# Kernel tuning notes

Measured on AMD Instinct MI355X. Metric: run time of the kernel, lower is better.

The kernel has to match this reference:

```python
import jax, jax.numpy as jnp
import numpy as np

D_MODEL = 1024
NUM_HEADS = 16
MAX_SEQ_LEN = 2048
THETA = 10000.0
D_K = D_MODEL // NUM_HEADS


def setup_inputs() -> dict:
    key = jax.random.key(0)
    ks = jax.random.split(key, 5)
    B, S = 4, MAX_SEQ_LEN
    std = 2.0 / (D_MODEL + D_MODEL)
    x = jax.random.normal(ks[0], (B, S, D_MODEL), dtype=jnp.float32)
    Wq = jax.random.normal(ks[1], (D_MODEL, D_MODEL), dtype=jnp.float32) * std
    Wk = jax.random.normal(ks[2], (D_MODEL, D_MODEL), dtype=jnp.float32) * std
    Wv = jax.random.normal(ks[3], (D_MODEL, D_MODEL), dtype=jnp.float32) * std
    Wo = jax.random.normal(ks[4], (D_MODEL, D_MODEL), dtype=jnp.float32) * std
    token_positions = jnp.arange(S, dtype=jnp.int64) if jax.config.jax_enable_x64 else jnp.arange(S, dtype=jnp.int32)
    return {"x": x, "token_positions": token_positions, "Wq": Wq, "Wk": Wk, "Wv": Wv, "Wo": Wo}


def _rope_tables(token_positions):
    # angles[i, j] = pos_i / theta^(2j/d_k),  j in [0, d_k/2)
    k = jnp.arange(0, D_K, 2, dtype=jnp.float32)
    inv_freq = 1.0 / (THETA ** (k / D_K))  # [d_k/2]
    angles = token_positions.astype(jnp.float32)[:, None] * inv_freq[None, :]  # [s, d_k/2]
    return jnp.sin(angles), jnp.cos(angles)


def _apply_rope(x, sin, cos):
    # x: [b, h, s, d_k], sin/cos: [s, d_k/2] broadcast over b,h
    x_even = x[..., 0::2]
    x_odd = x[..., 1::2]
    out_even = x_even * cos - x_odd * sin
    out_odd = x_odd * cos + x_even * sin
    # interleave back: [..., d_k/2, 2] -> [..., d_k]
    return jnp.stack([out_even, out_odd], axis=-1).reshape(x.shape)


def reference(x, token_positions, Wq, Wk, Wv, Wo):
    B, S, _ = x.shape
    H, Dk = NUM_HEADS, D_K

    def proj(W):
        y = jnp.einsum('oi,bsi->bso', W, x)
        return y.reshape(B, S, H, Dk).transpose(0, 2, 1, 3)  # [b, h, s, d_k]

    q, k, v = proj(Wq), proj(Wk), proj(Wv)
    sin, cos = _rope_tables(token_positions)
    q = _apply_rope(q, sin, cos)
    k = _apply_rope(k, sin, cos)

    scores = jnp.einsum('bhqd,bhkd->bhqk', q, k) / jnp.sqrt(jnp.float32(Dk))
    mask = jnp.tril(jnp.ones((S, S), dtype=bool))  # causal
    scores = jnp.where(mask[None, None], scores, -jnp.inf)
    attn = jax.nn.softmax(scores, axis=-1)
    out = jnp.einsum('bhqk,bhkd->bhqd', attn, v)
    out = out.transpose(0, 2, 1, 3).reshape(B, S, H * Dk)
    return jnp.einsum('oi,bsi->bso', Wo, out)
```

## Files before the change

kernel.cpp:

```cpp
#include <hip/hip_runtime.h>
#include <math.h>

#define S_LEN 2048
#define NHEADS 16
#define DK 64

typedef _Float16 h4 __attribute__((ext_vector_type(4)));
typedef _Float16 h8 __attribute__((ext_vector_type(8)));
typedef float f4 __attribute__((ext_vector_type(4)));

__device__ __forceinline__ void glds16(const void* g, void* l) {
  __builtin_amdgcn_global_load_lds(
      (const __attribute__((address_space(1))) unsigned int*)g,
      (__attribute__((address_space(3))) unsigned int*)l, 16, 0, 0);
}

__global__ void rope_table_kernel(const int* __restrict__ pos,
                                  float* __restrict__ sc) {
  int idx = blockIdx.x * blockDim.x + threadIdx.x;
  if (idx >= S_LEN * 32) return;
  int s = idx >> 5, p = idx & 31;
  double inv = pow(10000.0, -(double)(2 * p) / 64.0);
  double a = (double)pos[s] * inv;
  sc[s * 64 + 2 * p]     = (float)sin(a);
  sc[s * 64 + 2 * p + 1] = (float)cos(a);
}

__global__ __launch_bounds__(256) void cvt_all(
    const float* __restrict__ x,
    const float* __restrict__ w0, const float* __restrict__ w1,
    const float* __restrict__ w2, const float* __restrict__ w3,
    _Float16* __restrict__ xh, _Float16* __restrict__ wh) {
  int bid = blockIdx.x;
  if (bid < 8192) {
    int i = bid * 256 + threadIdx.x;
    float4 v = *(const float4*)(x + (size_t)i * 4);
    h4 o = {(_Float16)v.x, (_Float16)v.y, (_Float16)v.z, (_Float16)v.w};
    *(h4*)&xh[(size_t)i * 4] = o;
  } else {
    int j = (bid - 8192) * 256 + threadIdx.x;
    const float* srcs[4] = {w0, w1, w2, w3};
    int which = j >> 18;
    int off = (j & 262143) * 4;
    float4 v = *(const float4*)(srcs[which] + off);
    h4 o = {(_Float16)(v.x * 256.f), (_Float16)(v.y * 256.f),
            (_Float16)(v.z * 256.f), (_Float16)(v.w * 256.f)};
    *(h4*)&wh[(size_t)which * 1048576 + off] = o;
  }
}

__global__ __launch_bounds__(256) void gemm_qkv(
    const _Float16* __restrict__ A, const _Float16* __restrict__ W3,
    _Float16* __restrict__ Qo, _Float16* __restrict__ Ko,
    _Float16* __restrict__ Vto, const float* __restrict__ sc_t) {
  __shared__ _Float16 As[128 * 32];
  __shared__ _Float16 Bs[128 * 32];
  const int t = threadIdx.x;
  const int lane = t & 63;
  const int w = t >> 6;
  const int mat = blockIdx.x >> 3;
  const int n0 = (blockIdx.x & 7) * 128;
  const int m0 = blockIdx.y * 128;
  const _Float16* B = W3 + (size_t)mat * 1048576;
  const int wm = (w >> 1) * 64;
  const int wn = (w & 1) * 64;
  const int lm = lane & 15;
  const int kq = (lane >> 4) * 8;
  const int srow = lane >> 2;
  const int skof = (lane & 3) * 8;

  f4 acc[4][4];
#pragma unroll
  for (int i = 0; i < 4; i++)
#pragma unroll
    for (int j = 0; j < 4; j++) {
      f4 z = {0.f, 0.f, 0.f, 0.f};
      acc[i][j] = z;
    }

  for (int k0 = 0; k0 < 1024; k0 += 32) {
    __syncthreads();
#pragma unroll
    for (int c = 0; c < 2; c++) {
      int rr = (w + c * 4) * 16 + srow;
      glds16(A + (size_t)(m0 + rr) * 1024 + k0 + skof, (char*)As + (w + c * 4) * 1024);
      glds16(B + (size_t)(n0 + rr) * 1024 + k0 + skof, (char*)Bs + (w + c * 4) * 1024);
    }
    __syncthreads();

    h8 af[4], bf[4];
#pragma unroll
    for (int mt = 0; mt < 4; mt++)
      af[mt] = *(const h8*)(As + (wm + mt * 16 + lm) * 32 + kq);
#pragma unroll
    for (int nt = 0; nt < 4; nt++)
      bf[nt] = *(const h8*)(Bs + (wn + nt * 16 + lm) * 32 + kq);
#pragma unroll
    for (int mt = 0; mt < 4; mt++)
#pragma unroll
      for (int nt = 0; nt < 4; nt++)
        acc[mt][nt] = __builtin_amdgcn_mfma_f32_16x16x32_f16(af[mt], bf[nt],
                                                             acc[mt][nt], 0, 0, 0);
  }

  const float scale = 1.0f / 256.0f;
  const int quad = lane >> 4;
#pragma unroll
  for (int mt = 0; mt < 4; mt++) {
#pragma unroll
    for (int nt = 0; nt < 4; nt++) {
      int n = n0 + wn + nt * 16 + lm;
      int d = n & 63, h = n >> 6;
      int mbase = m0 + wm + mt * 16 + quad * 4;
      int s = mbase & (S_LEN - 1), b = mbase >> 11;
      if (mat == 2) {
        h4 ov = {(_Float16)(acc[mt][nt][0] * scale), (_Float16)(acc[mt][nt][1] * scale),
                 (_Float16)(acc[mt][nt][2] * scale), (_Float16)(acc[mt][nt][3] * scale)};
        *(h4*)&Vto[(((size_t)b * NHEADS + h) * DK + d) * S_LEN + s] = ov;
      } else {
        _Float16* C16 = (mat == 0) ? Qo : Ko;
        int p2 = d & ~1;
#pragma unroll
        for (int r = 0; r < 4; r++) {
          float v = acc[mt][nt][r] * scale;
          float2 sc = *(const float2*)&sc_t[(s + r) * 64 + p2];
          float partner = __shfl_xor(v, 1);
          v = (d & 1) ? fmaf(v, sc.y, partner * sc.x)
                      : fmaf(v, sc.y, -partner * sc.x);
          C16[(((size_t)b * NHEADS + h) * S_LEN + (s + r)) * DK + d] = (_Float16)v;
        }
      }
    }
  }
}

__global__ __launch_bounds__(256) void gemm_out(
    const _Float16* __restrict__ A, const _Float16* __restrict__ B,
    float* __restrict__ C32) {
  __shared__ _Float16 As[128 * 32];
  __shared__ _Float16 Bs[128 * 32];
  const int t = threadIdx.x;
  const int lane = t & 63;
  const int w = t >> 6;
  const int n0 = blockIdx.x * 128;
  const int m0 = blockIdx.y * 128;
  const int wm = (w >> 1) * 64;
  const int wn = (w & 1) * 64;
  const int lm = lane & 15;
  const int kq = (lane >> 4) * 8;
  const int srow = lane >> 2;
  const int skof = (lane & 3) * 8;

  f4 acc[4][4];
#pragma unroll
  for (int i = 0; i < 4; i++)
#pragma unroll
    for (int j = 0; j < 4; j++) {
      f4 z = {0.f, 0.f, 0.f, 0.f};
      acc[i][j] = z;
    }

  for (int k0 = 0; k0 < 1024; k0 += 32) {
    __syncthreads();
#pragma unroll
    for (int c = 0; c < 2; c++) {
      int rr = (w + c * 4) * 16 + srow;
      glds16(A + (size_t)(m0 + rr) * 1024 + k0 + skof, (char*)As + (w + c * 4) * 1024);
      glds16(B + (size_t)(n0 + rr) * 1024 + k0 + skof, (char*)Bs + (w + c * 4) * 1024);
    }
    __syncthreads();

    h8 af[4], bf[4];
#pragma unroll
    for (int mt = 0; mt < 4; mt++)
      af[mt] = *(const h8*)(As + (wm + mt * 16 + lm) * 32 + kq);
#pragma unroll
    for (int nt = 0; nt < 4; nt++)
      bf[nt] = *(const h8*)(Bs + (wn + nt * 16 + lm) * 32 + kq);
#pragma unroll
    for (int mt = 0; mt < 4; mt++)
#pragma unroll
      for (int nt = 0; nt < 4; nt++)
        acc[mt][nt] = __builtin_amdgcn_mfma_f32_16x16x32_f16(af[mt], bf[nt],
                                                             acc[mt][nt], 0, 0, 0);
  }

  const float scale = 1.0f / 256.0f;
  const int quad = lane >> 4;
#pragma unroll
  for (int mt = 0; mt < 4; mt++)
#pragma unroll
    for (int nt = 0; nt < 4; nt++) {
      int n = n0 + wn + nt * 16 + lm;
#pragma unroll
      for (int r = 0; r < 4; r++) {
        int m = m0 + wm + mt * 16 + quad * 4 + r;
        C32[(size_t)m * 1024 + n] = acc[mt][nt][r] * scale;
      }
    }
}

__global__ __launch_bounds__(256) void attn_mfma(
    const _Float16* __restrict__ Q, const _Float16* __restrict__ K,
    const _Float16* __restrict__ Vt, _Float16* __restrict__ O) {
  __shared__ _Float16 Ks[64 * 72];
  __shared__ _Float16 Vs[64 * 72];
  __shared__ _Float16 Ps[128 * 72];

  const int bh = blockIdx.x;
  const int qt = (gridDim.y - 1) - blockIdx.y;
  const int q0 = qt * 128;
  const int t = threadIdx.x;
  const int lane = t & 63;
  const int w = t >> 6;
  const int lm = lane & 15;
  const int quad = lane >> 4;
  const size_t qkbase = (size_t)bh * S_LEN * DK;
  const size_t vbase  = (size_t)bh * DK * S_LEN;
  const int srow = t >> 2;
  const int scol = (t & 3) * 16;
  const int wq0 = q0 + w * 32;

  h8 qf[2][2];
#pragma unroll
  for (int nt = 0; nt < 2; nt++)
#pragma unroll
    for (int kc = 0; kc < 2; kc++) {
      h8 v = *(const h8*)(Q + qkbase + (size_t)(wq0 + nt * 16 + lm) * DK +
                          kc * 32 + quad * 8);
#pragma unroll
      for (int j = 0; j < 8; j++) v[j] = v[j] * (_Float16)0.125f;
      qf[nt][kc] = v;
    }

  f4 oacc[4][2];
#pragma unroll
  for (int mt = 0; mt < 4; mt++)
#pragma unroll
    for (int nt = 0; nt < 2; nt++) {
      f4 z = {0.f, 0.f, 0.f, 0.f};
      oacc[mt][nt] = z;
    }
  float m_i[2] = {-INFINITY, -INFINITY};
  float l_i[2] = {0.f, 0.f};

  const int ktmax = 2 * qt + 1;
  const _Float16* kg = K + qkbase + (size_t)srow * DK + scol;
  const _Float16* vg = Vt + vbase + (size_t)srow * S_LEN + scol;
  h8 pk0 = *(const h8*)kg;
  h8 pk1 = *(const h8*)(kg + 8);
  h8 pv0 = *(const h8*)vg;
  h8 pv1 = *(const h8*)(vg + 8);

  for (int kt = 0; kt <= ktmax; kt++) {
    __syncthreads();
    *(h8*)&Ks[srow * 72 + scol] = pk0;
    *(h8*)&Ks[srow * 72 + scol + 8] = pk1;
    *(h8*)&Vs[srow * 72 + scol] = pv0;
    *(h8*)&Vs[srow * 72 + scol + 8] = pv1;
    if (kt < ktmax) {
      const _Float16* kgn = kg + (size_t)(kt + 1) * 64 * DK;
      const _Float16* vgn = vg + (kt + 1) * 64;
      pk0 = *(const h8*)kgn;
      pk1 = *(const h8*)(kgn + 8);
      pv0 = *(const h8*)vgn;
      pv1 = *(const h8*)(vgn + 8);
    }
    __syncthreads();

    if (kt * 64 <= wq0 + 31) {
      f4 s_[4][2];
#pragma unroll
      for (int mt = 0; mt < 4; mt++)
#pragma unroll
        for (int nt = 0; nt < 2; nt++) {
          f4 z = {0.f, 0.f, 0.f, 0.f};
          s_[mt][nt] = z;
        }
#pragma unroll
      for (int kc = 0; kc < 2; kc++) {
        h8 kf[4];
#pragma unroll
        for (int mt = 0; mt < 4; mt++)
          kf[mt] = *(const h8*)&Ks[(mt * 16 + lm) * 72 + kc * 32 + quad * 8];
#pragma unroll
        for (int mt = 0; mt < 4; mt++)
#pragma unroll
          for (int nt = 0; nt < 2; nt++)
            s_[mt][nt] = __builtin_amdgcn_mfma_f32_16x16x32_f16(kf[mt], qf[nt][kc],
                                                                s_[mt][nt], 0, 0, 0);
      }

      if (kt * 64 + 63 > wq0) {
#pragma unroll
        for (int nt = 0; nt < 2; nt++) {
          int srq = wq0 + nt * 16 + lm;
#pragma unroll
          for (int mt = 0; mt < 4; mt++)
#pragma unroll
            for (int r = 0; r < 4; r++)
              if (kt * 64 + mt * 16 + quad * 4 + r > srq) s_[mt][nt][r] = -INFINITY;
        }
      }

#pragma unroll
      for (int nt = 0; nt < 2; nt++) {
        float mx = -INFINITY;
#pragma unroll
        for (int mt = 0; mt < 4; mt++)
#pragma unroll
          for (int r = 0; r < 4; r++) mx = fmaxf(mx, s_[mt][nt][r]);
        mx = fmaxf(mx, __shfl_xor(mx, 16));
        mx = fmaxf(mx, __shfl_xor(mx, 32));
        const bool grow = __any(mx > m_i[nt]);
        const float mnew = grow ? fmaxf(m_i[nt], mx) : m_i[nt];
        float sum = 0.f;
#pragma unroll
        for (int mt = 0; mt < 4; mt++) {
          float p0 = __expf(s_[mt][nt][0] - mnew);
          float p1 = __expf(s_[mt][nt][1] - mnew);
          float p2 = __expf(s_[mt][nt][2] - mnew);
          float p3 = __expf(s_[mt][nt][3] - mnew);
          sum += (p0 + p1) + (p2 + p3);
          h4 pv = {(_Float16)p0, (_Float16)p1, (_Float16)p2, (_Float16)p3};
          *(h4*)&Ps[(w * 32 + nt * 16 + lm) * 72 + mt * 16 + quad * 4] = pv;
        }
        sum += __shfl_xor(sum, 16);
        sum += __shfl_xor(sum, 32);
        if (grow) {
          float alpha = __expf(m_i[nt] - mnew);
          m_i[nt] = mnew;
          l_i[nt] = fmaf(l_i[nt], alpha, sum);
#pragma unroll
          for (int mt = 0; mt < 4; mt++) {
            oacc[mt][nt][0] *= alpha; oacc[mt][nt][1] *= alpha;
            oacc[mt][nt][2] *= alpha; oacc[mt][nt][3] *= alpha;
          }
        } else {
          l_i[nt] += sum;
        }
      }

#pragma unroll
      for (int kc = 0; kc < 2; kc++) {
        h8 vf[4], pf[2];
#pragma unroll
        for (int mt = 0; mt < 4; mt++)
          vf[mt] = *(const h8*)&Vs[(mt * 16 + lm) * 72 + kc * 32 + quad * 8];
#pragma unroll
        for (int nt = 0; nt < 2; nt++)
          pf[nt] = *(const h8*)&Ps[(w * 32 + nt * 16 + lm) * 72 + kc * 32 + quad * 8];
#pragma unroll
        for (int mt = 0; mt < 4; mt++)
#pragma unroll
          for (int nt = 0; nt < 2; nt++)
            oacc[mt][nt] = __builtin_amdgcn_mfma_f32_16x16x32_f16(vf[mt], pf[nt],
                                                                  oacc[mt][nt], 0, 0, 0);
      }
    }
  }

  const int b = bh >> 4, head = bh & 15;
#pragma unroll
  for (int nt = 0; nt < 2; nt++) {
    float inv = 1.0f / l_i[nt];
    int s = wq0 + nt * 16 + lm;
#pragma unroll
    for (int mt = 0; mt < 4; mt++) {
      h4 ov = {(_Float16)(oacc[mt][nt][0] * inv), (_Float16)(oacc[mt][nt][1] * inv),
               (_Float16)(oacc[mt][nt][2] * inv), (_Float16)(oacc[mt][nt][3] * inv)};
      *(h4*)&O[((size_t)b * S_LEN + s) * 1024 + head * 64 + mt * 16 + quad * 4] = ov;
    }
  }
}

extern "C" void kernel_launch(void* const* d_in, const int* in_sizes, int n_in,
                              void* d_out, int out_size, void* d_ws, size_t ws_size,
                              hipStream_t stream) {
  const float* x   = (const float*)d_in[0];
  const int*   pos = (const int*)d_in[1];
  const float* Wq  = (const float*)d_in[2];
  const float* Wk  = (const float*)d_in[3];
  const float* Wv  = (const float*)d_in[4];
  const float* Wo  = (const float*)d_in[5];
  float* out = (float*)d_out;
  (void)in_sizes; (void)n_in; (void)out_size; (void)ws_size;

  const size_t NT = (size_t)4 * S_LEN * 1024;
  _Float16* q16  = (_Float16*)d_ws;
  _Float16* k16  = q16 + NT;
  _Float16* vt16 = k16 + NT;
  _Float16* aoh  = vt16 + NT;
  _Float16* xh   = aoh + NT;
  _Float16* wh   = xh + NT;
  float* sc_t = (float*)(wh + 4 * 1048576);

  rope_table_kernel<<<256, 256, 0, stream>>>(pos, sc_t);
  cvt_all<<<12288, 256, 0, stream>>>(x, Wq, Wk, Wv, Wo, xh, wh);

  gemm_qkv<<<dim3(24, 64), 256, 0, stream>>>(xh, wh, q16, k16, vt16, sc_t);

  attn_mfma<<<dim3(64, S_LEN / 128), 256, 0, stream>>>(q16, k16, vt16, aoh);

  gemm_out<<<dim3(8, 64), 256, 0, stream>>>(aoh, wh + 3145728, out);
}
```

Measured before the change: 277.4 us.

## Fuse rope table into convert kernel, swizzle attention LDS, shrink out-GEMM tile

Folds the rope sin/cos table computation into the conversion kernel as extra blocks, removing one launch. The attention kernel swaps its padded LDS rows (stride 72) for unpadded rows with an XOR swizzle, which shrinks LDS use, and adds an occupancy hint of 5 blocks per CU. The output GEMM moves from 128x128 to 64x128 tiles, doubling the grid to fill more CUs, at the cost of less B-tile reuse. The swizzle has to match exactly between the stores and the MFMA fragment reads.

```diff
diff --git a/kernel.cpp b/kernel.cpp
--- a/kernel.cpp
+++ b/kernel.cpp
@@ -15,29 +15,19 @@
       (__attribute__((address_space(3))) unsigned int*)l, 16, 0, 0);
 }
 
-__global__ void rope_table_kernel(const int* __restrict__ pos,
-                                  float* __restrict__ sc) {
-  int idx = blockIdx.x * blockDim.x + threadIdx.x;
-  if (idx >= S_LEN * 32) return;
-  int s = idx >> 5, p = idx & 31;
-  double inv = pow(10000.0, -(double)(2 * p) / 64.0);
-  double a = (double)pos[s] * inv;
-  sc[s * 64 + 2 * p]     = (float)sin(a);
-  sc[s * 64 + 2 * p + 1] = (float)cos(a);
-}
-
 __global__ __launch_bounds__(256) void cvt_all(
     const float* __restrict__ x,
     const float* __restrict__ w0, const float* __restrict__ w1,
     const float* __restrict__ w2, const float* __restrict__ w3,
-    _Float16* __restrict__ xh, _Float16* __restrict__ wh) {
+    _Float16* __restrict__ xh, _Float16* __restrict__ wh,
+    const int* __restrict__ pos, float* __restrict__ sc) {
   int bid = blockIdx.x;
   if (bid < 8192) {
     int i = bid * 256 + threadIdx.x;
     float4 v = *(const float4*)(x + (size_t)i * 4);
     h4 o = {(_Float16)v.x, (_Float16)v.y, (_Float16)v.z, (_Float16)v.w};
     *(h4*)&xh[(size_t)i * 4] = o;
-  } else {
+  } else if (bid < 12288) {
     int j = (bid - 8192) * 256 + threadIdx.x;
     const float* srcs[4] = {w0, w1, w2, w3};
     int which = j >> 18;
@@ -46,6 +36,13 @@
     h4 o = {(_Float16)(v.x * 256.f), (_Float16)(v.y * 256.f),
             (_Float16)(v.z * 256.f), (_Float16)(v.w * 256.f)};
     *(h4*)&wh[(size_t)which * 1048576 + off] = o;
+  } else {
+    int idx = (bid - 12288) * 256 + threadIdx.x;
+    int s = idx >> 5, p = idx & 31;
+    double inv = pow(10000.0, -(double)(2 * p) / 64.0);
+    double a = (double)pos[s] * inv;
+    sc[s * 64 + 2 * p]     = (float)sin(a);
+    sc[s * 64 + 2 * p + 1] = (float)cos(a);
   }
 }
 
@@ -137,23 +134,23 @@
 __global__ __launch_bounds__(256) void gemm_out(
     const _Float16* __restrict__ A, const _Float16* __restrict__ B,
     float* __restrict__ C32) {
-  __shared__ _Float16 As[128 * 32];
+  __shared__ _Float16 As[64 * 32];
   __shared__ _Float16 Bs[128 * 32];
   const int t = threadIdx.x;
   const int lane = t & 63;
   const int w = t >> 6;
   const int n0 = blockIdx.x * 128;
-  const int m0 = blockIdx.y * 128;
-  const int wm = (w >> 1) * 64;
+  const int m0 = blockIdx.y * 64;
+  const int wm = (w >> 1) * 32;
   const int wn = (w & 1) * 64;
   const int lm = lane & 15;
   const int kq = (lane >> 4) * 8;
   const int srow = lane >> 2;
   const int skof = (lane & 3) * 8;
 
-  f4 acc[4][4];
-#pragma unroll
-  for (int i = 0; i < 4; i++)
+  f4 acc[2][4];
+#pragma unroll
+  for (int i = 0; i < 2; i++)
 #pragma unroll
     for (int j = 0; j < 4; j++) {
       f4 z = {0.f, 0.f, 0.f, 0.f};
@@ -162,23 +159,23 @@
 
   for (int k0 = 0; k0 < 1024; k0 += 32) {
     __syncthreads();
+    glds16(A + (size_t)(m0 + w * 16 + srow) * 1024 + k0 + skof, (char*)As + w * 1024);
 #pragma unroll
     for (int c = 0; c < 2; c++) {
       int rr = (w + c * 4) * 16 + srow;
-      glds16(A + (size_t)(m0 + rr) * 1024 + k0 + skof, (char*)As + (w + c * 4) * 1024);
       glds16(B + (size_t)(n0 + rr) * 1024 + k0 + skof, (char*)Bs + (w + c * 4) * 1024);
     }
     __syncthreads();
 
-    h8 af[4], bf[4];
-#pragma unroll
-    for (int mt = 0; mt < 4; mt++)
+    h8 af[2], bf[4];
+#pragma unroll
+    for (int mt = 0; mt < 2; mt++)
       af[mt] = *(const h8*)(As + (wm + mt * 16 + lm) * 32 + kq);
 #pragma unroll
     for (int nt = 0; nt < 4; nt++)
       bf[nt] = *(const h8*)(Bs + (wn + nt * 16 + lm) * 32 + kq);
 #pragma unroll
-    for (int mt = 0; mt < 4; mt++)
+    for (int mt = 0; mt < 2; mt++)
 #pragma unroll
       for (int nt = 0; nt < 4; nt++)
         acc[mt][nt] = __builtin_amdgcn_mfma_f32_16x16x32_f16(af[mt], bf[nt],
@@ -188,7 +185,7 @@
   const float scale = 1.0f / 256.0f;
   const int quad = lane >> 4;
 #pragma unroll
-  for (int mt = 0; mt < 4; mt++)
+  for (int mt = 0; mt < 2; mt++)
 #pragma unroll
     for (int nt = 0; nt < 4; nt++) {
       int n = n0 + wn + nt * 16 + lm;
@@ -200,12 +197,12 @@
     }
 }
 
-__global__ __launch_bounds__(256) void attn_mfma(
+__global__ __launch_bounds__(256, 5) void attn_mfma(
     const _Float16* __restrict__ Q, const _Float16* __restrict__ K,
     const _Float16* __restrict__ Vt, _Float16* __restrict__ O) {
-  __shared__ _Float16 Ks[64 * 72];
-  __shared__ _Float16 Vs[64 * 72];
-  __shared__ _Float16 Ps[128 * 72];
+  __shared__ _Float16 Ks[64 * 64];
+  __shared__ _Float16 Vs[64 * 64];
+  __shared__ _Float16 Ps[128 * 64];
 
   const int bh = blockIdx.x;
   const int qt = (gridDim.y - 1) - blockIdx.y;
@@ -215,11 +212,19 @@
   const int w = t >> 6;
   const int lm = lane & 15;
   const int quad = lane >> 4;
+  const int l7 = lm & 7;
   const size_t qkbase = (size_t)bh * S_LEN * DK;
   const size_t vbase  = (size_t)bh * DK * S_LEN;
   const int srow = t >> 2;
   const int scol = (t & 3) * 16;
   const int wq0 = q0 + w * 32;
+  const f4 fzero = {0.f, 0.f, 0.f, 0.f};
+
+  const int r7 = srow & 7;
+  const int su0 = ((t & 3) * 2) ^ r7;
+  const int su1 = ((t & 3) * 2 + 1) ^ r7;
+  const int st0 = srow * 64 + su0 * 8;
+  const int st1 = srow * 64 + su1 * 8;
 
   h8 qf[2][2];
 #pragma unroll
@@ -237,10 +242,7 @@
 #pragma unroll
   for (int mt = 0; mt < 4; mt++)
 #pragma unroll
-    for (int nt = 0; nt < 2; nt++) {
-      f4 z = {0.f, 0.f, 0.f, 0.f};
-      oacc[mt][nt] = z;
-    }
+    for (int nt = 0; nt < 2; nt++) oacc[mt][nt] = fzero;
   float m_i[2] = {-INFINITY, -INFINITY};
   float l_i[2] = {0.f, 0.f};
 
@@ -254,10 +256,10 @@
 
   for (int kt = 0; kt <= ktmax; kt++) {
     __syncthreads();
-    *(h8*)&Ks[srow * 72 + scol] = pk0;
-    *(h8*)&Ks[srow * 72 + scol + 8] = pk1;
-    *(h8*)&Vs[srow * 72 + scol] = pv0;
-    *(h8*)&Vs[srow * 72 + scol + 8] = pv1;
+    *(h8*)&Ks[st0] = pk0;
+    *(h8*)&Ks[st1] = pk1;
+    *(h8*)&Vs[st0] = pv0;
+    *(h8*)&Vs[st1] = pv1;
     if (kt < ktmax) {
       const _Float16* kgn = kg + (size_t)(kt + 1) * 64 * DK;
       const _Float16* vgn = vg + (kt + 1) * 64;
@@ -270,24 +272,28 @@
 
     if (kt * 64 <= wq0 + 31) {
       f4 s_[4][2];
-#pragma unroll
-      for (int mt = 0; mt < 4; mt++)
-#pragma unroll
-        for (int nt = 0; nt < 2; nt++) {
-          f4 z = {0.f, 0.f, 0.f, 0.f};
-          s_[mt][nt] = z;
-        }
-#pragma unroll
-      for (int kc = 0; kc < 2; kc++) {
+      {
         h8 kf[4];
 #pragma unroll
         for (int mt = 0; mt < 4; mt++)
-          kf[mt] = *(const h8*)&Ks[(mt * 16 + lm) * 72 + kc * 32 + quad * 8];
+          kf[mt] = *(const h8*)&Ks[(mt * 16 + lm) * 64 + (quad ^ l7) * 8];
 #pragma unroll
         for (int mt = 0; mt < 4; mt++)
 #pragma unroll
           for (int nt = 0; nt < 2; nt++)
-            s_[mt][nt] = __builtin_amdgcn_mfma_f32_16x16x32_f16(kf[mt], qf[nt][kc],
+            s_[mt][nt] = __builtin_amdgcn_mfma_f32_16x16x32_f16(kf[mt], qf[nt][0],
+                                                                fzero, 0, 0, 0);
+      }
+      {
+        h8 kf[4];
+#pragma unroll
+        for (int mt = 0; mt < 4; mt++)
+          kf[mt] = *(const h8*)&Ks[(mt * 16 + lm) * 64 + ((4 + quad) ^ l7) * 8];
+#pragma unroll
+        for (int mt = 0; mt < 4; mt++)
+#pragma unroll
+          for (int nt = 0; nt < 2; nt++)
+            s_[mt][nt] = __builtin_amdgcn_mfma_f32_16x16x32_f16(kf[mt], qf[nt][1],
                                                                 s_[mt][nt], 0, 0, 0);
       }
 
@@ -315,6 +321,7 @@
         const bool grow = __any(mx > m_i[nt]);
         const float mnew = grow ? fmaxf(m_i[nt], mx) : m_i[nt];
         float sum = 0.f;
+        const int prow = (w * 32 + nt * 16 + lm) * 64;
 #pragma unroll
         for (int mt = 0; mt < 4; mt++) {
           float p0 = __expf(s_[mt][nt][0] - mnew);
@@ -323,7 +330,8 @@
           float p3 = __expf(s_[mt][nt][3] - mnew);
           sum += (p0 + p1) + (p2 + p3);
           h4 pv = {(_Float16)p0, (_Float16)p1, (_Float16)p2, (_Float16)p3};
-          *(h4*)&Ps[(w * 32 + nt * 16 + lm) * 72 + mt * 16 + quad * 4] = pv;
+          int pu = ((mt * 2 + (quad >> 1)) ^ l7) * 8 + (quad & 1) * 4;
+          *(h4*)&Ps[prow + pu] = pv;
         }
         sum += __shfl_xor(sum, 16);
         sum += __shfl_xor(sum, 32);
@@ -346,10 +354,11 @@
         h8 vf[4], pf[2];
 #pragma unroll
         for (int mt = 0; mt < 4; mt++)
-          vf[mt] = *(const h8*)&Vs[(mt * 16 + lm) * 72 + kc * 32 + quad * 8];
+          vf[mt] = *(const h8*)&Vs[(mt * 16 + lm) * 64 + ((kc * 4 + quad) ^ l7) * 8];
 #pragma unroll
         for (int nt = 0; nt < 2; nt++)
-          pf[nt] = *(const h8*)&Ps[(w * 32 + nt * 16 + lm) * 72 + kc * 32 + quad * 8];
+          pf[nt] = *(const h8*)&Ps[(w * 32 + nt * 16 + lm) * 64 +
+                                   ((kc * 4 + quad) ^ l7) * 8];
 #pragma unroll
         for (int mt = 0; mt < 4; mt++)
 #pragma unroll
@@ -395,12 +404,11 @@
   _Float16* wh   = xh + NT;
   float* sc_t = (float*)(wh + 4 * 1048576);
 
-  rope_table_kernel<<<256, 256, 0, stream>>>(pos, sc_t);
-  cvt_all<<<12288, 256, 0, stream>>>(x, Wq, Wk, Wv, Wo, xh, wh);
+  cvt_all<<<12544, 256, 0, stream>>>(x, Wq, Wk, Wv, Wo, xh, wh, pos, sc_t);
 
   gemm_qkv<<<dim3(24, 64), 256, 0, stream>>>(xh, wh, q16, k16, vt16, sc_t);
 
   attn_mfma<<<dim3(64, S_LEN / 128), 256, 0, stream>>>(q16, k16, vt16, aoh);
 
-  gemm_out<<<dim3(8, 64), 256, 0, stream>>>(aoh, wh + 3145728, out);
-}
+  gemm_out<<<dim3(8, 128), 256, 0, stream>>>(aoh, wh + 3145728, out);
+}
```

Measured after the change: 466.1 us. 68.1% more time.
